# Kernel tuning notes

Measured on AMD Instinct MI355X. Metric: run time of the kernel, lower is better.

Reference implementation:

```python
import jax, jax.numpy as jnp
import numpy as np

B, N, D, ATT = 8, 2048, 1024, 128

def setup_inputs() -> dict:
    key = jax.random.key(0)
    k1, k2, k3 = jax.random.split(key, 3)
    s = 1.0 / np.sqrt(D)
    return {
        "x": jax.random.normal(k1, (B, N, D), dtype=jnp.float32),
        "Wf": jax.random.normal(k2, (D, ATT), dtype=jnp.float32) * s,
        "bf": jnp.zeros((ATT,), dtype=jnp.float32),
        "Wg": jax.random.normal(k3, (D, ATT), dtype=jnp.float32) * s,
        "bg": jnp.zeros((ATT,), dtype=jnp.float32),
    }

def reference(x, Wf, bf, Wg, bg):
    # f, g: [B, N, ATT]
    f = jnp.einsum('bnd,da->bna', x, Wf) + bf
    g = jnp.einsum('bnd,da->bna', x, Wg) + bg
    # unscaled attention logits [B, N, N]
    att = jnp.einsum('bna,bma->bnm', f, g)
    att = jax.nn.softmax(att, axis=-1)
    # NOTE: original multiplies attention with x (not h); h branch is dead code.
    out = jnp.einsum('bnm,bmd->bnd', att, x)
    return out + x  # residual=True
```

## Files before the change

### kernel.cpp

```cpp
#include <hip/hip_runtime.h>
#include <hip/hip_fp16.h>


#define B_ 8
#define N_ 2048
#define D_ 1024
#define A_ 128

typedef _Float16 half8v  __attribute__((ext_vector_type(8)));
typedef _Float16 half4v  __attribute__((ext_vector_type(4)));
typedef float    floatx4 __attribute__((ext_vector_type(4)));

__device__ __forceinline__ floatx4 mfma_16x16x32(half8v a, half8v b, floatx4 c) {
#if defined(__HIP_DEVICE_COMPILE__)
    return __builtin_amdgcn_mfma_f32_16x16x32_f16(a, b, c, 0, 0, 0);
#else
    return c;
#endif
}
__device__ __forceinline__ floatx4 mfma_16x16x16(half4v a, half4v b, floatx4 c) {
#if defined(__HIP_DEVICE_COMPILE__)
    return __builtin_amdgcn_mfma_f32_16x16x16f16(a, b, c, 0, 0, 0);
#else
    return c;
#endif
}

__global__ __launch_bounds__(256) void xpose_kernel(
    const float* __restrict__ x, _Float16* __restrict__ xT)
{
    __shared__ __align__(16) _Float16 ts[64][80];
    const int n0 = blockIdx.x * 64, d0 = blockIdx.y * 64, b = blockIdx.z;
    const int t = threadIdx.x;
#pragma unroll
    for (int s = 0; s < 4; ++s) {
        int idx = t + 256 * s;
        int nl = idx >> 4, c4 = idx & 15;
        float4 v = ((const float4*)(x + ((size_t)(b * N_ + n0 + nl)) * D_ + d0))[c4];
        ts[c4 * 4 + 0][nl] = (_Float16)v.x;
        ts[c4 * 4 + 1][nl] = (_Float16)v.y;
        ts[c4 * 4 + 2][nl] = (_Float16)v.z;
        ts[c4 * 4 + 3][nl] = (_Float16)v.w;
    }
    __syncthreads();
#pragma unroll
    for (int s = 0; s < 2; ++s) {
        int idx = t + 256 * s;
        int dl = idx >> 3, c = idx & 7;
        *(uint4*)&xT[((size_t)b * D_ + d0 + dl) * N_ + n0 + c * 8] =
            *(const uint4*)&ts[dl][c * 8];
    }
}

__global__ __launch_bounds__(256) void wprep_kernel(
    const float* __restrict__ Wf, const float* __restrict__ Wg,
    _Float16* __restrict__ whT)
{
    __shared__ __align__(16) _Float16 ts[64][72];
    const int k0 = blockIdx.x * 64, c0 = blockIdx.y * 64;
    const float* W = blockIdx.z ? Wg : Wf;
    _Float16* dst = whT + (size_t)blockIdx.z * A_ * D_;
    const int t = threadIdx.x;
#pragma unroll
    for (int s = 0; s < 4; ++s) {
        int idx = t + 256 * s;
        int kl = idx >> 4, c4 = idx & 15;
        float4 v = *(const float4*)&W[(size_t)(k0 + kl) * A_ + c0 + c4 * 4];
        ts[c4 * 4 + 0][kl] = (_Float16)v.x;
        ts[c4 * 4 + 1][kl] = (_Float16)v.y;
        ts[c4 * 4 + 2][kl] = (_Float16)v.z;
        ts[c4 * 4 + 3][kl] = (_Float16)v.w;
    }
    __syncthreads();
#pragma unroll
    for (int s = 0; s < 2; ++s) {
        int idx = t + 256 * s;
        int cl = idx >> 3, ch = idx & 7;
        *(uint4*)&dst[(size_t)(c0 + cl) * D_ + k0 + ch * 8] =
            *(const uint4*)&ts[cl][ch * 8];
    }
}

__global__ __launch_bounds__(256) void fgmm_kernel(
    const float* __restrict__ x, const _Float16* __restrict__ whT,
    const float* __restrict__ bfv, const float* __restrict__ bgv,
    _Float16* __restrict__ fh, _Float16* __restrict__ gh)
{
    __shared__ __align__(16) _Float16 xs[64 * 48];
    __shared__ __align__(16) _Float16 wt[128 * 48];
    const int colh = blockIdx.x;
    const int row0 = blockIdx.y * 64;
    const int t = threadIdx.x;
    const int w = t >> 6, lane = t & 63, quad = lane >> 4, l16 = lane & 15;
    const int mtb = (w >> 1) * 32;
    const int wc  = (w & 1) * 64;

    float4 xR[2];
    uint4  wR[2];
#define FG_LOAD_TILE(K0)                                                      \
    {                                                                         \
        _Pragma("unroll")                                                     \
        for (int s = 0; s < 2; ++s) {                                         \
            int idx = t + 256 * s;                                            \
            int r = idx >> 3, c8 = idx & 7;                                   \
            xR[s] = *(const float4*)&x[(size_t)(row0 + r) * D_ + (K0) + c8 * 4]; \
        }                                                                     \
        _Pragma("unroll")                                                     \
        for (int s = 0; s < 2; ++s) {                                         \
            int idx = t + 256 * s;                                            \
            int c = idx >> 2, q = idx & 3;                                    \
            wR[s] = *(const uint4*)&whT[((size_t)(colh * A_ + c)) * D_ + (K0) + q * 8]; \
        }                                                                     \
    }

    FG_LOAD_TILE(0)

    floatx4 acc[2][4];
#pragma unroll
    for (int ms = 0; ms < 2; ++ms)
#pragma unroll
        for (int nt = 0; nt < 4; ++nt)
            acc[ms][nt] = (floatx4){0.f, 0.f, 0.f, 0.f};

    for (int kt = 0; kt < 32; ++kt) {
        __syncthreads();
#pragma unroll
        for (int s = 0; s < 2; ++s) {
            int idx = t + 256 * s;
            int r = idx >> 3, c8 = idx & 7;
            half4v h = {(_Float16)xR[s].x, (_Float16)xR[s].y,
                        (_Float16)xR[s].z, (_Float16)xR[s].w};
            *(half4v*)&xs[r * 48 + c8 * 4] = h;
        }
#pragma unroll
        for (int s = 0; s < 2; ++s) {
            int idx = t + 256 * s;
            int c = idx >> 2, q = idx & 3;
            *(uint4*)&wt[c * 48 + q * 8] = wR[s];
        }
        __syncthreads();
        if (kt < 31) FG_LOAD_TILE((kt + 1) * 32)

        half8v a0 = *(const half8v*)&xs[(mtb + l16) * 48 + quad * 8];
        half8v a1 = *(const half8v*)&xs[(mtb + 16 + l16) * 48 + quad * 8];
#pragma unroll
        for (int nt = 0; nt < 4; ++nt) {
            half8v bfr = *(const half8v*)&wt[(wc + nt * 16 + l16) * 48 + quad * 8];
            acc[0][nt] = mfma_16x16x32(a0, bfr, acc[0][nt]);
            acc[1][nt] = mfma_16x16x32(a1, bfr, acc[1][nt]);
        }
    }

    _Float16* dst = colh ? gh : fh;
    const float* bias = colh ? bgv : bfv;
#pragma unroll
    for (int nt = 0; nt < 4; ++nt) {
        int col = wc + nt * 16 + l16;
        float bv = bias[col];
#pragma unroll
        for (int ms = 0; ms < 2; ++ms)
#pragma unroll
            for (int rg = 0; rg < 4; ++rg) {
                int row = row0 + mtb + ms * 16 + quad * 4 + rg;
                dst[(size_t)row * A_ + col] = (_Float16)(acc[ms][nt][rg] + bv);
            }
    }
}

__global__ __launch_bounds__(256, 2) void attn_kernel(
    const float* __restrict__ x, const _Float16* __restrict__ f,
    const _Float16* __restrict__ g, const _Float16* __restrict__ xT,
    float* __restrict__ out)
{
    __shared__ __align__(16) _Float16 gS[32 * 136];
    __shared__ __align__(16) _Float16 xTs[256 * 40];

    const int dch = blockIdx.x;
    const int nt  = blockIdx.y;
    const int b   = blockIdx.z;
    const int tid = threadIdx.x;
    const int wave = tid >> 6, lane = tid & 63;
    const int quad = lane >> 4, l16 = lane & 15;
    const int d0 = dch * 256;
    const int qbase = nt * 128 + wave * 32;

    half8v fb[2][4];
#pragma unroll
    for (int it = 0; it < 2; ++it)
#pragma unroll
        for (int kc = 0; kc < 4; ++kc)
            fb[it][kc] = *(const half8v*)(f +
                ((size_t)(b * N_ + qbase + it * 16 + l16)) * A_ + kc * 32 + quad * 8);

    uint4 gR[2];
    uint2 xR[8];
#define AT_LOAD_TILE(M0)                                                      \
    {                                                                         \
        _Pragma("unroll")                                                     \
        for (int s = 0; s < 2; ++s) {                                         \
            int idx = tid + 256 * s;                                          \
            int r = idx >> 4, c = idx & 15;                                   \
            gR[s] = *(const uint4*)(g + ((size_t)(b * N_ + (M0) + r)) * A_ + c * 8); \
        }                                                                     \
        _Pragma("unroll")                                                     \
        for (int s = 0; s < 8; ++s) {                                         \
            int idx = tid + 256 * s;                                          \
            int rr = idx >> 3, p = idx & 7;                                   \
            int kp = ((p & 1) << 4) + (p >> 1) * 4;                           \
            xR[s] = *(const uint2*)(xT + ((size_t)b * D_ + d0 + rr) * N_ + (M0) + kp); \
        }                                                                     \
    }

    AT_LOAD_TILE(0)

    floatx4 acc[2][16];
#pragma unroll
    for (int it = 0; it < 2; ++it)
#pragma unroll
        for (int dt = 0; dt < 16; ++dt)
            acc[it][dt] = (floatx4){0.f, 0.f, 0.f, 0.f};
    float m_i[2] = {-3.0e38f, -3.0e38f};
    float l_i[2] = {0.f, 0.f};

    for (int m0 = 0; m0 < N_; m0 += 32) {
        __syncthreads();
#pragma unroll
        for (int s = 0; s < 2; ++s) {
            int idx = tid + 256 * s;
            int r = idx >> 4, c = idx & 15;
            *(uint4*)&gS[r * 136 + c * 8] = gR[s];
        }
#pragma unroll
        for (int s = 0; s < 8; ++s) {
            int idx = tid + 256 * s;
            int rr = idx >> 3, p = idx & 7;
            *(uint2*)&xTs[rr * 40 + p * 4] = xR[s];
        }
        __syncthreads();
        if (m0 + 32 < N_) AT_LOAD_TILE(m0 + 32)

        floatx4 sc[2][2];
#pragma unroll
        for (int jt = 0; jt < 2; ++jt)
#pragma unroll
            for (int it = 0; it < 2; ++it)
                sc[jt][it] = (floatx4){0.f, 0.f, 0.f, 0.f};
#pragma unroll
        for (int kc = 0; kc < 4; ++kc) {
            half8v ga0 = *(const half8v*)&gS[(l16     ) * 136 + kc * 32 + quad * 8];
            half8v ga1 = *(const half8v*)&gS[(l16 + 16) * 136 + kc * 32 + quad * 8];
            sc[0][0] = mfma_16x16x32(ga0, fb[0][kc], sc[0][0]);
            sc[0][1] = mfma_16x16x32(ga0, fb[1][kc], sc[0][1]);
            sc[1][0] = mfma_16x16x32(ga1, fb[0][kc], sc[1][0]);
            sc[1][1] = mfma_16x16x32(ga1, fb[1][kc], sc[1][1]);
        }

        float tm[2];
#pragma unroll
        for (int it = 0; it < 2; ++it) {
            float t0 = fmaxf(fmaxf(sc[0][it][0], sc[0][it][1]),
                             fmaxf(sc[0][it][2], sc[0][it][3]));
            float t1 = fmaxf(fmaxf(sc[1][it][0], sc[1][it][1]),
                             fmaxf(sc[1][it][2], sc[1][it][3]));
            float tv = fmaxf(t0, t1);
            tv = fmaxf(tv, __shfl_xor(tv, 16));
            tv = fmaxf(tv, __shfl_xor(tv, 32));
            tm[it] = tv;
        }
        bool needl = (tm[0] > m_i[0] + 8.0f) || (tm[1] > m_i[1] + 8.0f);
        if (__any(needl)) {
            float alpha[2];
#pragma unroll
            for (int it = 0; it < 2; ++it) {
                float mnew = fmaxf(m_i[it], tm[it]);
                alpha[it] = __expf(m_i[it] - mnew);
                m_i[it] = mnew;
                l_i[it] *= alpha[it];
            }
            float ar[2][4];
#pragma unroll
            for (int it = 0; it < 2; ++it)
#pragma unroll
                for (int r = 0; r < 4; ++r)
                    ar[it][r] = __shfl(alpha[it], quad * 4 + r);
#pragma unroll
            for (int it = 0; it < 2; ++it)
#pragma unroll
                for (int dt = 0; dt < 16; ++dt)
#pragma unroll
                    for (int r = 0; r < 4; ++r)
                        acc[it][dt][r] *= ar[it][r];
        }

        half4v pa[2][2];
#pragma unroll
        for (int it = 0; it < 2; ++it) {
            float rs = 0.f;
#pragma unroll
            for (int jt = 0; jt < 2; ++jt) {
                float p0 = __expf(sc[jt][it][0] - m_i[it]);
                float p1 = __expf(sc[jt][it][1] - m_i[it]);
                float p2 = __expf(sc[jt][it][2] - m_i[it]);
                float p3 = __expf(sc[jt][it][3] - m_i[it]);
                rs += (p0 + p1) + (p2 + p3);
                pa[jt][it] = (half4v){(_Float16)p0, (_Float16)p1,
                                      (_Float16)p2, (_Float16)p3};
            }
            rs += __shfl_xor(rs, 16);
            rs += __shfl_xor(rs, 32);
            l_i[it] += rs;
        }

#pragma unroll
        for (int dt = 0; dt < 16; ++dt) {
            half8v xb = *(const half8v*)&xTs[(dt * 16 + l16) * 40 + quad * 8];
            half4v xb0 = __builtin_shufflevector(xb, xb, 0, 1, 2, 3);
            half4v xb1 = __builtin_shufflevector(xb, xb, 4, 5, 6, 7);
            acc[0][dt] = mfma_16x16x16(pa[0][0], xb0, acc[0][dt]);
            acc[0][dt] = mfma_16x16x16(pa[1][0], xb1, acc[0][dt]);
            acc[1][dt] = mfma_16x16x16(pa[0][1], xb0, acc[1][dt]);
            acc[1][dt] = mfma_16x16x16(pa[1][1], xb1, acc[1][dt]);
        }
    }

    float linv[2][4];
#pragma unroll
    for (int it = 0; it < 2; ++it)
#pragma unroll
        for (int r = 0; r < 4; ++r)
            linv[it][r] = 1.0f / __shfl(l_i[it], quad * 4 + r);

#pragma unroll
    for (int it = 0; it < 2; ++it)
#pragma unroll
        for (int r = 0; r < 4; ++r) {
            const size_t rowoff =
                ((size_t)(b * N_ + qbase + it * 16 + quad * 4 + r)) * D_ + d0;
#pragma unroll
            for (int dt = 0; dt < 16; ++dt) {
                int col = dt * 16 + l16;
                out[rowoff + col] = fmaf(acc[it][dt][r], linv[it][r], x[rowoff + col]);
            }
        }
}

extern "C" void kernel_launch(void* const* d_in, const int* in_sizes, int n_in,
                              void* d_out, int out_size, void* d_ws, size_t ws_size,
                              hipStream_t stream) {
    const float* x   = (const float*)d_in[0];
    const float* Wf  = (const float*)d_in[1];
    const float* bfv = (const float*)d_in[2];
    const float* Wg  = (const float*)d_in[3];
    const float* bgv = (const float*)d_in[4];
    float* out = (float*)d_out;

    _Float16* fh  = (_Float16*)d_ws;
    _Float16* gh  = fh + (size_t)B_ * N_ * A_;
    _Float16* xT  = gh + (size_t)B_ * N_ * A_;
    _Float16* whT = xT + (size_t)B_ * D_ * N_;

    hipLaunchKernelGGL(xpose_kernel, dim3(N_ / 64, D_ / 64, B_), dim3(256), 0, stream,
                       x, xT);
    hipLaunchKernelGGL(wprep_kernel, dim3(D_ / 64, A_ / 64, 2), dim3(256), 0, stream,
                       Wf, Wg, whT);
    hipLaunchKernelGGL(fgmm_kernel, dim3(2, B_ * N_ / 64), dim3(256), 0, stream,
                       x, whT, bfv, bgv, fh, gh);
    hipLaunchKernelGGL(attn_kernel, dim3(D_ / 256, N_ / 128, B_), dim3(256), 0, stream,
                       x, fh, gh, xT, out);
}
```

Measured before the change: 350.6 us.

## Widen attention key tile to 64 and fuse f/g projections per block

The attention kernel now processes 64 keys per iteration instead of 32. It permutes g rows in shared memory so the softmax probabilities map directly onto 16x16x32 MFMA operands, which replaces the 16x16x16 MFMAs in the PV product. The row-sum shuffle reduction moves out of the loop and happens once at the end. The f/g projection kernel now computes both projections in one block, so each x tile is loaded and converted once instead of twice. The cost is more shared memory and registers, which could lower occupancy.

```diff
diff --git a/kernel.cpp b/kernel.cpp
--- a/kernel.cpp
+++ b/kernel.cpp
@@ -11,16 +11,9 @@
 typedef _Float16 half4v  __attribute__((ext_vector_type(4)));
 typedef float    floatx4 __attribute__((ext_vector_type(4)));
 
-__device__ __forceinline__ floatx4 mfma_16x16x32(half8v a, half8v b, floatx4 c) {
+__device__ __forceinline__ floatx4 mfma32(half8v a, half8v b, floatx4 c) {
 #if defined(__HIP_DEVICE_COMPILE__)
     return __builtin_amdgcn_mfma_f32_16x16x32_f16(a, b, c, 0, 0, 0);
-#else
-    return c;
-#endif
-}
-__device__ __forceinline__ floatx4 mfma_16x16x16(half4v a, half4v b, floatx4 c) {
-#if defined(__HIP_DEVICE_COMPILE__)
-    return __builtin_amdgcn_mfma_f32_16x16x16f16(a, b, c, 0, 0, 0);
 #else
     return c;
 #endif
@@ -86,40 +79,39 @@
     const float* __restrict__ bfv, const float* __restrict__ bgv,
     _Float16* __restrict__ fh, _Float16* __restrict__ gh)
 {
-    __shared__ __align__(16) _Float16 xs[64 * 48];
-    __shared__ __align__(16) _Float16 wt[128 * 48];
-    const int colh = blockIdx.x;
-    const int row0 = blockIdx.y * 64;
+    __shared__ __align__(16) _Float16 xs[64 * 40];
+    __shared__ __align__(16) _Float16 wt[256 * 40];
+    const int row0 = blockIdx.x * 64;
     const int t = threadIdx.x;
     const int w = t >> 6, lane = t & 63, quad = lane >> 4, l16 = lane & 15;
-    const int mtb = (w >> 1) * 32;
-    const int wc  = (w & 1) * 64;
-
-    float4 xR[2];
-    uint4  wR[2];
+    const int wr  = (w >> 1) * 32;
+    const int wch = (w & 1);
+
+    float4 xRf[2];
+    uint4  wR[4];
 #define FG_LOAD_TILE(K0)                                                      \
     {                                                                         \
         _Pragma("unroll")                                                     \
         for (int s = 0; s < 2; ++s) {                                         \
             int idx = t + 256 * s;                                            \
-            int r = idx >> 3, c8 = idx & 7;                                   \
-            xR[s] = *(const float4*)&x[(size_t)(row0 + r) * D_ + (K0) + c8 * 4]; \
+            int r = idx >> 3, k4 = idx & 7;                                   \
+            xRf[s] = *(const float4*)&x[(size_t)(row0 + r) * D_ + (K0) + k4 * 4]; \
         }                                                                     \
         _Pragma("unroll")                                                     \
-        for (int s = 0; s < 2; ++s) {                                         \
+        for (int s = 0; s < 4; ++s) {                                         \
             int idx = t + 256 * s;                                            \
-            int c = idx >> 2, q = idx & 3;                                    \
-            wR[s] = *(const uint4*)&whT[((size_t)(colh * A_ + c)) * D_ + (K0) + q * 8]; \
+            int c = idx >> 2, k8 = idx & 3;                                   \
+            wR[s] = *(const uint4*)&whT[(size_t)c * D_ + (K0) + k8 * 8];      \
         }                                                                     \
     }
 
     FG_LOAD_TILE(0)
 
-    floatx4 acc[2][4];
+    floatx4 acc[2][8];
 #pragma unroll
     for (int ms = 0; ms < 2; ++ms)
 #pragma unroll
-        for (int nt = 0; nt < 4; ++nt)
+        for (int nt = 0; nt < 8; ++nt)
             acc[ms][nt] = (floatx4){0.f, 0.f, 0.f, 0.f};
 
     for (int kt = 0; kt < 32; ++kt) {
@@ -127,41 +119,41 @@
 #pragma unroll
         for (int s = 0; s < 2; ++s) {
             int idx = t + 256 * s;
-            int r = idx >> 3, c8 = idx & 7;
-            half4v h = {(_Float16)xR[s].x, (_Float16)xR[s].y,
-                        (_Float16)xR[s].z, (_Float16)xR[s].w};
-            *(half4v*)&xs[r * 48 + c8 * 4] = h;
-        }
-#pragma unroll
-        for (int s = 0; s < 2; ++s) {
+            int r = idx >> 3, k4 = idx & 7;
+            half4v h = {(_Float16)xRf[s].x, (_Float16)xRf[s].y,
+                        (_Float16)xRf[s].z, (_Float16)xRf[s].w};
+            *(half4v*)&xs[r * 40 + k4 * 4] = h;
+        }
+#pragma unroll
+        for (int s = 0; s < 4; ++s) {
             int idx = t + 256 * s;
-            int c = idx >> 2, q = idx & 3;
-            *(uint4*)&wt[c * 48 + q * 8] = wR[s];
+            int c = idx >> 2, k8 = idx & 3;
+            *(uint4*)&wt[c * 40 + k8 * 8] = wR[s];
         }
         __syncthreads();
         if (kt < 31) FG_LOAD_TILE((kt + 1) * 32)
 
-        half8v a0 = *(const half8v*)&xs[(mtb + l16) * 48 + quad * 8];
-        half8v a1 = *(const half8v*)&xs[(mtb + 16 + l16) * 48 + quad * 8];
-#pragma unroll
-        for (int nt = 0; nt < 4; ++nt) {
-            half8v bfr = *(const half8v*)&wt[(wc + nt * 16 + l16) * 48 + quad * 8];
-            acc[0][nt] = mfma_16x16x32(a0, bfr, acc[0][nt]);
-            acc[1][nt] = mfma_16x16x32(a1, bfr, acc[1][nt]);
-        }
-    }
-
-    _Float16* dst = colh ? gh : fh;
-    const float* bias = colh ? bgv : bfv;
-#pragma unroll
-    for (int nt = 0; nt < 4; ++nt) {
-        int col = wc + nt * 16 + l16;
+        half8v a0 = *(const half8v*)&xs[(wr + l16) * 40 + quad * 8];
+        half8v a1 = *(const half8v*)&xs[(wr + 16 + l16) * 40 + quad * 8];
+#pragma unroll
+        for (int nt = 0; nt < 8; ++nt) {
+            half8v bfr = *(const half8v*)&wt[(wch * 128 + nt * 16 + l16) * 40 + quad * 8];
+            acc[0][nt] = mfma32(a0, bfr, acc[0][nt]);
+            acc[1][nt] = mfma32(a1, bfr, acc[1][nt]);
+        }
+    }
+
+    _Float16* dst = wch ? gh : fh;
+    const float* bias = wch ? bgv : bfv;
+#pragma unroll
+    for (int nt = 0; nt < 8; ++nt) {
+        int col = nt * 16 + l16;
         float bv = bias[col];
 #pragma unroll
         for (int ms = 0; ms < 2; ++ms)
 #pragma unroll
             for (int rg = 0; rg < 4; ++rg) {
-                int row = row0 + mtb + ms * 16 + quad * 4 + rg;
+                int row = row0 + wr + ms * 16 + quad * 4 + rg;
                 dst[(size_t)row * A_ + col] = (_Float16)(acc[ms][nt][rg] + bv);
             }
     }
@@ -172,8 +164,8 @@
     const _Float16* __restrict__ g, const _Float16* __restrict__ xT,
     float* __restrict__ out)
 {
-    __shared__ __align__(16) _Float16 gS[32 * 136];
-    __shared__ __align__(16) _Float16 xTs[256 * 40];
+    __shared__ __align__(16) _Float16 gS[64 * 136];
+    __shared__ __align__(16) _Float16 xTs[256 * 72];
 
     const int dch = blockIdx.x;
     const int nt  = blockIdx.y;
@@ -192,12 +184,12 @@
             fb[it][kc] = *(const half8v*)(f +
                 ((size_t)(b * N_ + qbase + it * 16 + l16)) * A_ + kc * 32 + quad * 8);
 
-    uint4 gR[2];
-    uint2 xR[8];
+    uint4 gR[4];
+    uint4 xR[8];
 #define AT_LOAD_TILE(M0)                                                      \
     {                                                                         \
         _Pragma("unroll")                                                     \
-        for (int s = 0; s < 2; ++s) {                                         \
+        for (int s = 0; s < 4; ++s) {                                         \
             int idx = tid + 256 * s;                                          \
             int r = idx >> 4, c = idx & 15;                                   \
             gR[s] = *(const uint4*)(g + ((size_t)(b * N_ + (M0) + r)) * A_ + c * 8); \
@@ -205,9 +197,8 @@
         _Pragma("unroll")                                                     \
         for (int s = 0; s < 8; ++s) {                                         \
             int idx = tid + 256 * s;                                          \
-            int rr = idx >> 3, p = idx & 7;                                   \
-            int kp = ((p & 1) << 4) + (p >> 1) * 4;                           \
-            xR[s] = *(const uint2*)(xT + ((size_t)b * D_ + d0 + rr) * N_ + (M0) + kp); \
+            int rr = idx >> 3, jc = idx & 7;                                  \
+            xR[s] = *(const uint4*)(xT + ((size_t)b * D_ + d0 + rr) * N_ + (M0) + jc * 8); \
         }                                                                     \
     }
 
@@ -219,50 +210,58 @@
 #pragma unroll
         for (int dt = 0; dt < 16; ++dt)
             acc[it][dt] = (floatx4){0.f, 0.f, 0.f, 0.f};
-    float m_i[2] = {-3.0e38f, -3.0e38f};
-    float l_i[2] = {0.f, 0.f};
-
-    for (int m0 = 0; m0 < N_; m0 += 32) {
+    float m_i[2]    = {-3.0e38f, -3.0e38f};
+    float l_part[2] = {0.f, 0.f};
+
+    for (int m0 = 0; m0 < N_; m0 += 64) {
         __syncthreads();
 #pragma unroll
-        for (int s = 0; s < 2; ++s) {
+        for (int s = 0; s < 4; ++s) {
             int idx = tid + 256 * s;
             int r = idx >> 4, c = idx & 15;
-            *(uint4*)&gS[r * 136 + c * 8] = gR[s];
+            int slot = (r & 32) + ((r >> 2) & 1) * 16 + ((r >> 3) & 3) * 4 + (r & 3);
+            *(uint4*)&gS[slot * 136 + c * 8] = gR[s];
         }
 #pragma unroll
         for (int s = 0; s < 8; ++s) {
             int idx = tid + 256 * s;
-            int rr = idx >> 3, p = idx & 7;
-            *(uint2*)&xTs[rr * 40 + p * 4] = xR[s];
+            int rr = idx >> 3, jc = idx & 7;
+            *(uint4*)&xTs[rr * 72 + jc * 8] = xR[s];
         }
         __syncthreads();
-        if (m0 + 32 < N_) AT_LOAD_TILE(m0 + 32)
-
-        floatx4 sc[2][2];
-#pragma unroll
-        for (int jt = 0; jt < 2; ++jt)
-#pragma unroll
-            for (int it = 0; it < 2; ++it)
-                sc[jt][it] = (floatx4){0.f, 0.f, 0.f, 0.f};
-#pragma unroll
-        for (int kc = 0; kc < 4; ++kc) {
-            half8v ga0 = *(const half8v*)&gS[(l16     ) * 136 + kc * 32 + quad * 8];
-            half8v ga1 = *(const half8v*)&gS[(l16 + 16) * 136 + kc * 32 + quad * 8];
-            sc[0][0] = mfma_16x16x32(ga0, fb[0][kc], sc[0][0]);
-            sc[0][1] = mfma_16x16x32(ga0, fb[1][kc], sc[0][1]);
-            sc[1][0] = mfma_16x16x32(ga1, fb[0][kc], sc[1][0]);
-            sc[1][1] = mfma_16x16x32(ga1, fb[1][kc], sc[1][1]);
-        }
+        if (m0 + 64 < N_) AT_LOAD_TILE(m0 + 64)
+
+        floatx4 sc[2][2][2];
+#pragma unroll
+        for (int kb = 0; kb < 2; ++kb)
+#pragma unroll
+            for (int fr = 0; fr < 2; ++fr)
+#pragma unroll
+                for (int it = 0; it < 2; ++it)
+                    sc[kb][fr][it] = (floatx4){0.f, 0.f, 0.f, 0.f};
+#pragma unroll
+        for (int kc = 0; kc < 4; ++kc)
+#pragma unroll
+            for (int kb = 0; kb < 2; ++kb) {
+                half8v ga0 = *(const half8v*)&gS[(kb * 32 + l16) * 136 + kc * 32 + quad * 8];
+                half8v ga1 = *(const half8v*)&gS[(kb * 32 + 16 + l16) * 136 + kc * 32 + quad * 8];
+                sc[kb][0][0] = mfma32(ga0, fb[0][kc], sc[kb][0][0]);
+                sc[kb][0][1] = mfma32(ga0, fb[1][kc], sc[kb][0][1]);
+                sc[kb][1][0] = mfma32(ga1, fb[0][kc], sc[kb][1][0]);
+                sc[kb][1][1] = mfma32(ga1, fb[1][kc], sc[kb][1][1]);
+            }
 
         float tm[2];
 #pragma unroll
         for (int it = 0; it < 2; ++it) {
-            float t0 = fmaxf(fmaxf(sc[0][it][0], sc[0][it][1]),
-                             fmaxf(sc[0][it][2], sc[0][it][3]));
-            float t1 = fmaxf(fmaxf(sc[1][it][0], sc[1][it][1]),
-                             fmaxf(sc[1][it][2], sc[1][it][3]));
-            float tv = fmaxf(t0, t1);
+            float tv = -3.0e38f;
+#pragma unroll
+            for (int kb = 0; kb < 2; ++kb)
+#pragma unroll
+                for (int fr = 0; fr < 2; ++fr)
+#pragma unroll
+                    for (int r = 0; r < 4; ++r)
+                        tv = fmaxf(tv, sc[kb][fr][it][r]);
             tv = fmaxf(tv, __shfl_xor(tv, 16));
             tv = fmaxf(tv, __shfl_xor(tv, 32));
             tm[it] = tv;
@@ -275,7 +274,7 @@
                 float mnew = fmaxf(m_i[it], tm[it]);
                 alpha[it] = __expf(m_i[it] - mnew);
                 m_i[it] = mnew;
-                l_i[it] *= alpha[it];
+                l_part[it] *= alpha[it];
             }
             float ar[2][4];
 #pragma unroll
@@ -292,37 +291,48 @@
                         acc[it][dt][r] *= ar[it][r];
         }
 
-        half4v pa[2][2];
+        half8v pa[2][2];
 #pragma unroll
         for (int it = 0; it < 2; ++it) {
             float rs = 0.f;
 #pragma unroll
-            for (int jt = 0; jt < 2; ++jt) {
-                float p0 = __expf(sc[jt][it][0] - m_i[it]);
-                float p1 = __expf(sc[jt][it][1] - m_i[it]);
-                float p2 = __expf(sc[jt][it][2] - m_i[it]);
-                float p3 = __expf(sc[jt][it][3] - m_i[it]);
-                rs += (p0 + p1) + (p2 + p3);
-                pa[jt][it] = (half4v){(_Float16)p0, (_Float16)p1,
-                                      (_Float16)p2, (_Float16)p3};
-            }
-            rs += __shfl_xor(rs, 16);
-            rs += __shfl_xor(rs, 32);
-            l_i[it] += rs;
+            for (int kb = 0; kb < 2; ++kb) {
+                float e0 = __expf(sc[kb][0][it][0] - m_i[it]);
+                float e1 = __expf(sc[kb][0][it][1] - m_i[it]);
+                float e2 = __expf(sc[kb][0][it][2] - m_i[it]);
+                float e3 = __expf(sc[kb][0][it][3] - m_i[it]);
+                float e4 = __expf(sc[kb][1][it][0] - m_i[it]);
+                float e5 = __expf(sc[kb][1][it][1] - m_i[it]);
+                float e6 = __expf(sc[kb][1][it][2] - m_i[it]);
+                float e7 = __expf(sc[kb][1][it][3] - m_i[it]);
+                rs += ((e0 + e1) + (e2 + e3)) + ((e4 + e5) + (e6 + e7));
+                pa[kb][it] = (half8v){(_Float16)e0, (_Float16)e1, (_Float16)e2,
+                                      (_Float16)e3, (_Float16)e4, (_Float16)e5,
+                                      (_Float16)e6, (_Float16)e7};
+            }
+            l_part[it] += rs;
         }
 
 #pragma unroll
         for (int dt = 0; dt < 16; ++dt) {
-            half8v xb = *(const half8v*)&xTs[(dt * 16 + l16) * 40 + quad * 8];
-            half4v xb0 = __builtin_shufflevector(xb, xb, 0, 1, 2, 3);
-            half4v xb1 = __builtin_shufflevector(xb, xb, 4, 5, 6, 7);
-            acc[0][dt] = mfma_16x16x16(pa[0][0], xb0, acc[0][dt]);
-            acc[0][dt] = mfma_16x16x16(pa[1][0], xb1, acc[0][dt]);
-            acc[1][dt] = mfma_16x16x16(pa[0][1], xb0, acc[1][dt]);
-            acc[1][dt] = mfma_16x16x16(pa[1][1], xb1, acc[1][dt]);
-        }
-    }
-
+            const int ro = (dt * 16 + l16) * 72;
+            half8v xb0 = *(const half8v*)&xTs[ro + quad * 8];
+            half8v xb1 = *(const half8v*)&xTs[ro + 32 + quad * 8];
+            acc[0][dt] = mfma32(pa[0][0], xb0, acc[0][dt]);
+            acc[0][dt] = mfma32(pa[1][0], xb1, acc[0][dt]);
+            acc[1][dt] = mfma32(pa[0][1], xb0, acc[1][dt]);
+            acc[1][dt] = mfma32(pa[1][1], xb1, acc[1][dt]);
+        }
+    }
+
+    float l_i[2];
+#pragma unroll
+    for (int it = 0; it < 2; ++it) {
+        float rs = l_part[it];
+        rs += __shfl_xor(rs, 16);
+        rs += __shfl_xor(rs, 32);
+        l_i[it] = rs;
+    }
     float linv[2][4];
 #pragma unroll
     for (int it = 0; it < 2; ++it)
@@ -363,7 +373,7 @@
                        x, xT);
     hipLaunchKernelGGL(wprep_kernel, dim3(D_ / 64, A_ / 64, 2), dim3(256), 0, stream,
                        Wf, Wg, whT);
-    hipLaunchKernelGGL(fgmm_kernel, dim3(2, B_ * N_ / 64), dim3(256), 0, stream,
+    hipLaunchKernelGGL(fgmm_kernel, dim3(B_ * N_ / 64), dim3(256), 0, stream,
                        x, whT, bfv, bgv, fh, gh);
     hipLaunchKernelGGL(attn_kernel, dim3(D_ / 256, N_ / 128, B_), dim3(256), 0, stream,
                        x, fh, gh, xT, out);
```

After: 539.1 us. 1.54x slower.
